# Optimization experiments

Measured on AMD Instinct MI355X. Metric: run time of the kernel, lower is better.

Reference implementation:

```python
import jax, jax.numpy as jnp
import numpy as np


def setup_inputs() -> dict:
    key = jax.random.key(0)
    k1, k2, k3 = jax.random.split(key, 3)
    N, M, D = 8192, 8192, 128
    feat = jax.random.normal(k1, (N, D), dtype=jnp.float32)
    feat2 = jax.random.normal(k2, (M, D), dtype=jnp.float32)
    labels = jax.random.randint(k3, (N,), 0, M, dtype=jnp.int64)
    temp = jnp.array(1.0, dtype=jnp.float32)
    return {"feat": feat, "feat2": feat2, "temp": temp, "labels": labels}


def reference(feat, feat2, temp, labels):
    # (same math as sqrt(sum((x[:,None]-y)**2, -1)) but without the N*M*D intermediate).
    x_sq = jnp.sum(feat * feat, axis=-1)    # [N]
    y_sq = jnp.sum(feat2 * feat2, axis=-1)  # [M]
    sq_dist = x_sq[:, None] + y_sq[None, :] - 2.0 * (feat @ feat2.T)  # [N, M]
    dist = jnp.sqrt(jnp.maximum(sq_dist, 0.0))
    logits = -temp * dist                    # [N, M]
    # Cross-entropy with mean reduction (nn.CrossEntropyLoss default)
    log_z = jax.nn.logsumexp(logits, axis=-1)                              # [N]
    picked = jnp.take_along_axis(logits, labels[:, None], axis=1)[:, 0]   # [N]
    return jnp.mean(log_z - picked)
```

## Files before the change

kernel.cpp:

```cpp
#include <hip/hip_runtime.h>
#include <hip/hip_bf16.h>
#include <stdint.h>

#define NR 8192
#define MC 8192
#define DD 128
#define MSPLIT 16
#define CPB 512
#define TILES 16
#define ROWBLK 128

typedef __attribute__((ext_vector_type(8))) short short8;
typedef __attribute__((ext_vector_type(16))) float f32x16;

__device__ __forceinline__ ushort bf16r(float f) {
    __hip_bfloat16 h = __float2bfloat16(f);
    return *(ushort*)&h;
}

__device__ __forceinline__ void gload_lds16(const void* g, void* l) {
    __builtin_amdgcn_global_load_lds(
        (const __attribute__((address_space(1))) uint32_t*)g,
        (__attribute__((address_space(3))) uint32_t*)l, 16, 0, 0);
}
__device__ __forceinline__ void gload_lds4(const void* g, void* l) {
    __builtin_amdgcn_global_load_lds(
        (const __attribute__((address_space(1))) uint32_t*)g,
        (__attribute__((address_space(3))) uint32_t*)l, 4, 0, 0);
}

__global__ __launch_bounds__(256) void prep_kernel(
    const float* __restrict__ feat, const float* __restrict__ feat2,
    const float* __restrict__ temp_p, const int* __restrict__ labels,
    ushort* __restrict__ fb, ushort* __restrict__ f2bf,
    float* __restrict__ xsq2, float* __restrict__ ysq2,
    float* __restrict__ pick, float* __restrict__ consts) {
    int b = blockIdx.x;
    if (b < 2048) {
        int row = b * 4 + (threadIdx.x >> 6);
        int l = threadIdx.x & 63;
        float temp = *temp_p;
        float c = temp * 1.4426950408889634f;
        float c2 = c * c;
        int lab = labels[row];
        float2 x = ((const float2*)(feat  + (size_t)row * DD))[l];
        float2 y = ((const float2*)(feat2 + (size_t)row * DD))[l];
        float2 z = ((const float2*)(feat2 + (size_t)lab * DD))[l];
        ushort2 ux; ux.x = bf16r(x.x); ux.y = bf16r(x.y);
        ((ushort2*)(fb + (size_t)row * DD))[l] = ux;
        float sx = x.x * x.x + x.y * x.y;
        float sy = y.x * y.x + y.y * y.y;
        float d0 = x.x - z.x, d1 = x.y - z.y;
        float sd = d0 * d0 + d1 * d1;
        #pragma unroll
        for (int off = 1; off < 64; off <<= 1) {
            sx += __shfl_xor(sx, off);
            sy += __shfl_xor(sy, off);
            sd += __shfl_xor(sd, off);
        }
        if (l == 0) {
            xsq2[row] = c2 * sx;
            ysq2[row] = c2 * sy;
            pick[row] = temp * __builtin_amdgcn_sqrtf(sd);
            if (row == 0) consts[0] = -2.0f * c2;
        }
    } else {
        int id = (b - 2048) * 256 + threadIdx.x;
        int slot = id & 63;
        int ks = (id >> 6) & 7;
        int tile = id >> 9;
        int col = tile * 32 + (slot & 31);
        int k0 = ks * 16 + (slot >> 5) * 8;
        const float* src = feat2 + (size_t)col * DD + k0;
        float4 v0 = ((const float4*)src)[0];
        float4 v1 = ((const float4*)src)[1];
        short8 o;
        o[0] = (short)bf16r(v0.x); o[1] = (short)bf16r(v0.y);
        o[2] = (short)bf16r(v0.z); o[3] = (short)bf16r(v0.w);
        o[4] = (short)bf16r(v1.x); o[5] = (short)bf16r(v1.y);
        o[6] = (short)bf16r(v1.z); o[7] = (short)bf16r(v1.w);
        ((short8*)f2bf)[id] = o;
    }
}

__global__ __launch_bounds__(256, 4) void main_kernel(
    const ushort* __restrict__ fb, const ushort* __restrict__ f2bf,
    const float* __restrict__ xsq2, const float* __restrict__ ysq2,
    const float* __restrict__ consts, float* __restrict__ spart) {
    __shared__ ushort lds[4][8 * 512];
    __shared__ float ys_lds[CPB];

    int bid = blockIdx.x;
    int cs = bid & (MSPLIT - 1);
    int rb = bid >> 4;
    int tid = threadIdx.x;
    int wave = tid >> 6, lane = tid & 63;
    int lcol = lane & 31, lhalf = lane >> 5;
    int rowbase = rb * ROWBLK + wave * 32;
    int tile0 = cs * TILES;
    float m2c2 = consts[0];

    short8 a[8];
    const ushort* ap = fb + (size_t)(rowbase + lcol) * DD + lhalf * 8;
    #pragma unroll
    for (int ks = 0; ks < 8; ++ks) a[ks] = *(const short8*)(ap + ks * 16);

    float xs2[16];
    #pragma unroll
    for (int r = 0; r < 16; ++r)
        xs2[r] = xsq2[rowbase + (r & 3) + 8 * (r >> 2) + 4 * lhalf];

    float s[16];
    #pragma unroll
    for (int r = 0; r < 16; ++r) s[r] = 0.f;

    {
        const float* ysrc = ysq2 + cs * CPB;
        gload_lds4(ysrc + wave * 64 + lane, &ys_lds[wave * 64]);
        gload_lds4(ysrc + (wave + 4) * 64 + lane, &ys_lds[(wave + 4) * 64]);
    }
    #pragma unroll
    for (int t0 = 0; t0 < 2; ++t0) {
        const ushort* g = f2bf + ((size_t)(tile0 + t0) * 8 + wave) * 512 + lane * 8;
        gload_lds16(g, &lds[t0][wave * 512]);
        gload_lds16(g + 4 * 512, &lds[t0][(wave + 4) * 512]);
    }

    #pragma unroll 1
    for (int t = 0; t < TILES; ++t) {
        if (t + 2 < TILES) {
            const ushort* g = f2bf + ((size_t)(tile0 + t + 2) * 8 + wave) * 512 + lane * 8;
            gload_lds16(g, &lds[(t + 2) & 3][wave * 512]);
            gload_lds16(g + 4 * 512, &lds[(t + 2) & 3][(wave + 4) * 512]);
            asm volatile("s_waitcnt vmcnt(4)" ::: "memory");
        } else if (t + 1 < TILES) {
            asm volatile("s_waitcnt vmcnt(2)" ::: "memory");
        } else {
            asm volatile("s_waitcnt vmcnt(0)" ::: "memory");
        }
        __builtin_amdgcn_s_barrier();

        float ysv = ys_lds[t * 32 + lcol];
        const ushort* lb = &lds[t & 3][0];
        f32x16 acc;
        #pragma unroll
        for (int r = 0; r < 16; ++r) acc[r] = 0.f;
        #pragma unroll
        for (int ks = 0; ks < 8; ++ks) {
            short8 bf = *(const short8*)(lb + ks * 512 + lane * 8);
            acc = __builtin_amdgcn_mfma_f32_32x32x16_bf16(a[ks], bf, acc, 0, 0, 0);
        }
        #pragma unroll
        for (int r = 0; r < 16; ++r) {
            float q = fmaxf(fmaf(m2c2, acc[r], xs2[r] + ysv), 0.f);
            s[r] += __builtin_amdgcn_exp2f(-__builtin_amdgcn_sqrtf(q));
        }
    }

    #pragma unroll
    for (int off = 1; off <= 16; off <<= 1)
        #pragma unroll
        for (int r = 0; r < 16; ++r) s[r] += __shfl_xor(s[r], off);

    if (lcol == 0) {
        float* sp = spart + (size_t)cs * NR + rowbase;
        #pragma unroll
        for (int r = 0; r < 16; ++r)
            sp[(r & 3) + 8 * (r >> 2) + 4 * lhalf] = s[r];
    }
}

__global__ __launch_bounds__(256) void finish1_kernel(
    const float* __restrict__ spart, const float* __restrict__ pick,
    float* __restrict__ partial) {
    __shared__ float red[4];
    int row = blockIdx.x * 256 + threadIdx.x;
    float ssum = 0.f;
    #pragma unroll
    for (int ms = 0; ms < MSPLIT; ++ms) ssum += spart[(size_t)ms * NR + row];
    float v = __builtin_amdgcn_logf(ssum) * 0.6931471805599453f + pick[row];
    #pragma unroll
    for (int off = 1; off < 64; off <<= 1) v += __shfl_xor(v, off);
    if ((threadIdx.x & 63) == 0) red[threadIdx.x >> 6] = v;
    __syncthreads();
    if (threadIdx.x == 0) partial[blockIdx.x] = red[0] + red[1] + red[2] + red[3];
}

__global__ void finish2_kernel(const float* __restrict__ partial, float* __restrict__ out) {
    float v = (threadIdx.x < 32) ? partial[threadIdx.x] : 0.f;
    #pragma unroll
    for (int off = 1; off < 64; off <<= 1) v += __shfl_xor(v, off);
    if (threadIdx.x == 0) out[0] = v * (1.0f / NR);
}

extern "C" void kernel_launch(void* const* d_in, const int* in_sizes, int n_in,
                              void* d_out, int out_size, void* d_ws, size_t ws_size,
                              hipStream_t stream) {
    const float* feat   = (const float*)d_in[0];
    const float* feat2  = (const float*)d_in[1];
    const float* temp   = (const float*)d_in[2];
    const int*   labels = (const int*)d_in[3];
    float* out = (float*)d_out;

    char* ws = (char*)d_ws;
    ushort* fb    = (ushort*)ws;
    ushort* f2bf  = (ushort*)(ws + (2u << 20));
    float*  xsq2  = (float*)(ws + (4u << 20));
    float*  ysq2  = xsq2 + NR;
    float*  pick  = ysq2 + MC;
    float*  consts  = pick + NR;
    float*  partial = consts + 16;
    float*  spart = (float*)(ws + (5u << 20));

    prep_kernel<<<2560, 256, 0, stream>>>(feat, feat2, temp, labels,
                                          fb, f2bf, xsq2, ysq2, pick, consts);
    main_kernel<<<(NR / ROWBLK) * MSPLIT, 256, 0, stream>>>(fb, f2bf, xsq2, ysq2, consts, spart);
    finish1_kernel<<<NR / 256, 256, 0, stream>>>(spart, pick, partial);
    finish2_kernel<<<1, 64, 0, stream>>>(partial, out);
}
```

Baseline: 44.02 us.

## Fuse final reductions into main kernel via last-block atomic; process two tiles per iteration

Removes the two finish kernels: each main-kernel block bumps an atomic counter after writing its partial sums, and the last block to finish does the logsumexp reduction and writes the output. The spart layout becomes row-major so that block can read the 16 splits per row with float4 loads. The tile loop also now handles two tiles per barrier with two independent MFMA accumulators, waiting on vmcnt(0) and issuing the next pair of prefetches after the barrier. This trades two kernel launches and finer-grained load/compute overlap for a serial tail reduction in one block and atomic/fence overhead.

```diff
diff --git a/kernel.cpp b/kernel.cpp
--- a/kernel.cpp
+++ b/kernel.cpp
@@ -9,6 +9,7 @@
 #define CPB 512
 #define TILES 16
 #define ROWBLK 128
+#define GRID ((NR / ROWBLK) * MSPLIT)
 
 typedef __attribute__((ext_vector_type(8))) short short8;
 typedef __attribute__((ext_vector_type(16))) float f32x16;
@@ -34,8 +35,9 @@
     const float* __restrict__ temp_p, const int* __restrict__ labels,
     ushort* __restrict__ fb, ushort* __restrict__ f2bf,
     float* __restrict__ xsq2, float* __restrict__ ysq2,
-    float* __restrict__ pick, float* __restrict__ consts) {
+    float* __restrict__ pick, float* __restrict__ consts, int* __restrict__ done) {
     int b = blockIdx.x;
+    if (b == 0 && threadIdx.x == 0) *done = 0;
     if (b < 2048) {
         int row = b * 4 + (threadIdx.x >> 6);
         int l = threadIdx.x & 63;
@@ -86,9 +88,12 @@
 __global__ __launch_bounds__(256, 4) void main_kernel(
     const ushort* __restrict__ fb, const ushort* __restrict__ f2bf,
     const float* __restrict__ xsq2, const float* __restrict__ ysq2,
-    const float* __restrict__ consts, float* __restrict__ spart) {
+    const float* __restrict__ consts, float* __restrict__ spart,
+    const float* __restrict__ pick, int* __restrict__ done, float* __restrict__ out) {
     __shared__ ushort lds[4][8 * 512];
     __shared__ float ys_lds[CPB];
+    __shared__ float red[4];
+    __shared__ int last_flag;
 
     int bid = blockIdx.x;
     int cs = bid & (MSPLIT - 1);
@@ -118,42 +123,54 @@
         const float* ysrc = ysq2 + cs * CPB;
         gload_lds4(ysrc + wave * 64 + lane, &ys_lds[wave * 64]);
         gload_lds4(ysrc + (wave + 4) * 64 + lane, &ys_lds[(wave + 4) * 64]);
-    }
-    #pragma unroll
-    for (int t0 = 0; t0 < 2; ++t0) {
-        const ushort* g = f2bf + ((size_t)(tile0 + t0) * 8 + wave) * 512 + lane * 8;
-        gload_lds16(g, &lds[t0][wave * 512]);
-        gload_lds16(g + 4 * 512, &lds[t0][(wave + 4) * 512]);
+        #pragma unroll
+        for (int t0 = 0; t0 < 2; ++t0) {
+            const ushort* g = f2bf + ((size_t)(tile0 + t0) * 8 + wave) * 512 + lane * 8;
+            gload_lds16(g, &lds[t0][wave * 512]);
+            gload_lds16(g + 4 * 512, &lds[t0][(wave + 4) * 512]);
+        }
     }
 
     #pragma unroll 1
-    for (int t = 0; t < TILES; ++t) {
-        if (t + 2 < TILES) {
-            const ushort* g = f2bf + ((size_t)(tile0 + t + 2) * 8 + wave) * 512 + lane * 8;
-            gload_lds16(g, &lds[(t + 2) & 3][wave * 512]);
-            gload_lds16(g + 4 * 512, &lds[(t + 2) & 3][(wave + 4) * 512]);
-            asm volatile("s_waitcnt vmcnt(4)" ::: "memory");
-        } else if (t + 1 < TILES) {
-            asm volatile("s_waitcnt vmcnt(2)" ::: "memory");
-        } else {
-            asm volatile("s_waitcnt vmcnt(0)" ::: "memory");
-        }
+    for (int j = 0; j < TILES / 2; ++j) {
+        asm volatile("s_waitcnt vmcnt(0)" ::: "memory");
         __builtin_amdgcn_s_barrier();
 
-        float ysv = ys_lds[t * 32 + lcol];
-        const ushort* lb = &lds[t & 3][0];
-        f32x16 acc;
-        #pragma unroll
-        for (int r = 0; r < 16; ++r) acc[r] = 0.f;
+        if (j + 1 < TILES / 2) {
+            #pragma unroll
+            for (int p = 0; p < 2; ++p) {
+                int t = 2 * j + 2 + p;
+                const ushort* g = f2bf + ((size_t)(tile0 + t) * 8 + wave) * 512 + lane * 8;
+                gload_lds16(g, &lds[t & 3][wave * 512]);
+                gload_lds16(g + 4 * 512, &lds[t & 3][(wave + 4) * 512]);
+            }
+        }
+
+        int t0 = 2 * j, t1 = 2 * j + 1;
+        float ysv0 = ys_lds[t0 * 32 + lcol];
+        float ysv1 = ys_lds[t1 * 32 + lcol];
+        const ushort* lb0 = &lds[t0 & 3][0];
+        const ushort* lb1 = &lds[t1 & 3][0];
+
+        f32x16 acc0, acc1;
+        #pragma unroll
+        for (int r = 0; r < 16; ++r) { acc0[r] = 0.f; acc1[r] = 0.f; }
         #pragma unroll
         for (int ks = 0; ks < 8; ++ks) {
-            short8 bf = *(const short8*)(lb + ks * 512 + lane * 8);
-            acc = __builtin_amdgcn_mfma_f32_32x32x16_bf16(a[ks], bf, acc, 0, 0, 0);
+            short8 b0 = *(const short8*)(lb0 + ks * 512 + lane * 8);
+            acc0 = __builtin_amdgcn_mfma_f32_32x32x16_bf16(a[ks], b0, acc0, 0, 0, 0);
+        }
+        #pragma unroll
+        for (int ks = 0; ks < 8; ++ks) {
+            short8 b1 = *(const short8*)(lb1 + ks * 512 + lane * 8);
+            acc1 = __builtin_amdgcn_mfma_f32_32x32x16_bf16(a[ks], b1, acc1, 0, 0, 0);
         }
         #pragma unroll
         for (int r = 0; r < 16; ++r) {
-            float q = fmaxf(fmaf(m2c2, acc[r], xs2[r] + ysv), 0.f);
-            s[r] += __builtin_amdgcn_exp2f(-__builtin_amdgcn_sqrtf(q));
+            float q0 = fmaxf(fmaf(m2c2, acc0[r], xs2[r] + ysv0), 0.f);
+            float q1 = fmaxf(fmaf(m2c2, acc1[r], xs2[r] + ysv1), 0.f);
+            s[r] += __builtin_amdgcn_exp2f(-__builtin_amdgcn_sqrtf(q0));
+            s[r] += __builtin_amdgcn_exp2f(-__builtin_amdgcn_sqrtf(q1));
         }
     }
 
@@ -163,34 +180,35 @@
         for (int r = 0; r < 16; ++r) s[r] += __shfl_xor(s[r], off);
 
     if (lcol == 0) {
-        float* sp = spart + (size_t)cs * NR + rowbase;
         #pragma unroll
         for (int r = 0; r < 16; ++r)
-            sp[(r & 3) + 8 * (r >> 2) + 4 * lhalf] = s[r];
-    }
-}
-
-__global__ __launch_bounds__(256) void finish1_kernel(
-    const float* __restrict__ spart, const float* __restrict__ pick,
-    float* __restrict__ partial) {
-    __shared__ float red[4];
-    int row = blockIdx.x * 256 + threadIdx.x;
-    float ssum = 0.f;
-    #pragma unroll
-    for (int ms = 0; ms < MSPLIT; ++ms) ssum += spart[(size_t)ms * NR + row];
-    float v = __builtin_amdgcn_logf(ssum) * 0.6931471805599453f + pick[row];
-    #pragma unroll
-    for (int off = 1; off < 64; off <<= 1) v += __shfl_xor(v, off);
-    if ((threadIdx.x & 63) == 0) red[threadIdx.x >> 6] = v;
+            spart[(size_t)(rowbase + (r & 3) + 8 * (r >> 2) + 4 * lhalf) * MSPLIT + cs] = s[r];
+    }
+
+    __threadfence();
+    if (tid == 0) last_flag = (atomicAdd(done, 1) == GRID - 1);
     __syncthreads();
-    if (threadIdx.x == 0) partial[blockIdx.x] = red[0] + red[1] + red[2] + red[3];
-}
-
-__global__ void finish2_kernel(const float* __restrict__ partial, float* __restrict__ out) {
-    float v = (threadIdx.x < 32) ? partial[threadIdx.x] : 0.f;
-    #pragma unroll
-    for (int off = 1; off < 64; off <<= 1) v += __shfl_xor(v, off);
-    if (threadIdx.x == 0) out[0] = v * (1.0f / NR);
+    if (!last_flag) return;
+    __threadfence();
+
+    float local = 0.f;
+    #pragma unroll 1
+    for (int k = 0; k < NR / 256; ++k) {
+        int row = k * 256 + tid;
+        const float4* sp = (const float4*)(spart + (size_t)row * MSPLIT);
+        float4 p0 = sp[0], p1 = sp[1], p2 = sp[2], p3 = sp[3];
+        float ssum = (((((((((((((((p0.x + p0.y) + p0.z) + p0.w) + p1.x) + p1.y) + p1.z)
+                     + p1.w) + p2.x) + p2.y) + p2.z) + p2.w) + p3.x) + p3.y) + p3.z) + p3.w);
+        local += __builtin_amdgcn_logf(ssum) * 0.6931471805599453f + pick[row];
+    }
+    #pragma unroll
+    for (int off = 1; off < 64; off <<= 1) local += __shfl_xor(local, off);
+    if ((tid & 63) == 0) red[tid >> 6] = local;
+    __syncthreads();
+    if (tid == 0) {
+        out[0] = (red[0] + red[1] + red[2] + red[3]) * (1.0f / NR);
+        *done = 0;
+    }
 }
 
 extern "C" void kernel_launch(void* const* d_in, const int* in_sizes, int n_in,
@@ -209,12 +227,11 @@
     float*  ysq2  = xsq2 + NR;
     float*  pick  = ysq2 + MC;
     float*  consts  = pick + NR;
-    float*  partial = consts + 16;
+    int*    done    = (int*)(consts + 16);
     float*  spart = (float*)(ws + (5u << 20));
 
     prep_kernel<<<2560, 256, 0, stream>>>(feat, feat2, temp, labels,
-                                          fb, f2bf, xsq2, ysq2, pick, consts);
-    main_kernel<<<(NR / ROWBLK) * MSPLIT, 256, 0, stream>>>(fb, f2bf, xsq2, ysq2, consts, spart);
-    finish1_kernel<<<NR / 256, 256, 0, stream>>>(spart, pick, partial);
-    finish2_kernel<<<1, 64, 0, stream>>>(partial, out);
-}
+                                          fb, f2bf, xsq2, ysq2, pick, consts, done);
+    main_kernel<<<GRID, 256, 0, stream>>>(fb, f2bf, xsq2, ysq2, consts, spart,
+                                          pick, done, out);
+}
```

After: 140.5 us. +219.2%, slower.

## Shrink main kernel blocks to two waves with double-buffered B tiles

Applied to the files above, without the earlier changes.

Halves the row block to 64 rows and the main kernel block to 128 threads, which doubles the grid and halves LDS per block. The four-deep prefetch ring becomes a two-buffer scheme: each iteration waits for all loads, hits a barrier, then issues the next tile. Wave priority is raised around the MFMA loop, and the clamp to zero before sqrt becomes an fabs. The aim is more resident blocks and better latency hiding from extra parallelism, but each B tile is now reloaded by twice as many blocks and the prefetch lead is shorter.

```diff
diff --git a/kernel.cpp b/kernel.cpp
--- a/kernel.cpp
+++ b/kernel.cpp
@@ -8,7 +8,8 @@
 #define MSPLIT 16
 #define CPB 512
 #define TILES 16
-#define ROWBLK 128
+#define ROWBLK 64
+#define GRID ((NR / ROWBLK) * MSPLIT)
 
 typedef __attribute__((ext_vector_type(8))) short short8;
 typedef __attribute__((ext_vector_type(16))) float f32x16;
@@ -83,11 +84,11 @@
     }
 }
 
-__global__ __launch_bounds__(256, 4) void main_kernel(
+__global__ __launch_bounds__(128, 4) void main_kernel(
     const ushort* __restrict__ fb, const ushort* __restrict__ f2bf,
     const float* __restrict__ xsq2, const float* __restrict__ ysq2,
     const float* __restrict__ consts, float* __restrict__ spart) {
-    __shared__ ushort lds[4][8 * 512];
+    __shared__ ushort lds[2][8 * 512];
     __shared__ float ys_lds[CPB];
 
     int bid = blockIdx.x;
@@ -116,44 +117,48 @@
 
     {
         const float* ysrc = ysq2 + cs * CPB;
-        gload_lds4(ysrc + wave * 64 + lane, &ys_lds[wave * 64]);
-        gload_lds4(ysrc + (wave + 4) * 64 + lane, &ys_lds[(wave + 4) * 64]);
-    }
-    #pragma unroll
-    for (int t0 = 0; t0 < 2; ++t0) {
-        const ushort* g = f2bf + ((size_t)(tile0 + t0) * 8 + wave) * 512 + lane * 8;
-        gload_lds16(g, &lds[t0][wave * 512]);
-        gload_lds16(g + 4 * 512, &lds[t0][(wave + 4) * 512]);
+        #pragma unroll
+        for (int c = 0; c < 4; ++c) {
+            int ch = wave * 4 + c;
+            gload_lds4(ysrc + ch * 64 + lane, &ys_lds[ch * 64]);
+        }
+        #pragma unroll
+        for (int c = 0; c < 4; ++c) {
+            int ch = wave * 4 + c;
+            gload_lds16(f2bf + ((size_t)tile0 * 8 + ch) * 512 + lane * 8,
+                        &lds[0][ch * 512]);
+        }
     }
 
     #pragma unroll 1
     for (int t = 0; t < TILES; ++t) {
-        if (t + 2 < TILES) {
-            const ushort* g = f2bf + ((size_t)(tile0 + t + 2) * 8 + wave) * 512 + lane * 8;
-            gload_lds16(g, &lds[(t + 2) & 3][wave * 512]);
-            gload_lds16(g + 4 * 512, &lds[(t + 2) & 3][(wave + 4) * 512]);
-            asm volatile("s_waitcnt vmcnt(4)" ::: "memory");
-        } else if (t + 1 < TILES) {
-            asm volatile("s_waitcnt vmcnt(2)" ::: "memory");
-        } else {
-            asm volatile("s_waitcnt vmcnt(0)" ::: "memory");
-        }
+        asm volatile("s_waitcnt vmcnt(0)" ::: "memory");
         __builtin_amdgcn_s_barrier();
+        if (t + 1 < TILES) {
+            #pragma unroll
+            for (int c = 0; c < 4; ++c) {
+                int ch = wave * 4 + c;
+                gload_lds16(f2bf + ((size_t)(tile0 + t + 1) * 8 + ch) * 512 + lane * 8,
+                            &lds[(t + 1) & 1][ch * 512]);
+            }
+        }
 
         float ysv = ys_lds[t * 32 + lcol];
-        const ushort* lb = &lds[t & 3][0];
+        const ushort* lb = &lds[t & 1][0];
         f32x16 acc;
         #pragma unroll
         for (int r = 0; r < 16; ++r) acc[r] = 0.f;
+        __builtin_amdgcn_s_setprio(1);
         #pragma unroll
         for (int ks = 0; ks < 8; ++ks) {
             short8 bf = *(const short8*)(lb + ks * 512 + lane * 8);
             acc = __builtin_amdgcn_mfma_f32_32x32x16_bf16(a[ks], bf, acc, 0, 0, 0);
         }
+        __builtin_amdgcn_s_setprio(0);
         #pragma unroll
         for (int r = 0; r < 16; ++r) {
-            float q = fmaxf(fmaf(m2c2, acc[r], xs2[r] + ysv), 0.f);
-            s[r] += __builtin_amdgcn_exp2f(-__builtin_amdgcn_sqrtf(q));
+            float q = fmaf(m2c2, acc[r], xs2[r] + ysv);
+            s[r] += __builtin_amdgcn_exp2f(-__builtin_amdgcn_sqrtf(__builtin_fabsf(q)));
         }
     }
 
@@ -214,7 +219,7 @@
 
     prep_kernel<<<2560, 256, 0, stream>>>(feat, feat2, temp, labels,
                                           fb, f2bf, xsq2, ysq2, pick, consts);
-    main_kernel<<<(NR / ROWBLK) * MSPLIT, 256, 0, stream>>>(fb, f2bf, xsq2, ysq2, consts, spart);
+    main_kernel<<<GRID, 128, 0, stream>>>(fb, f2bf, xsq2, ysq2, consts, spart);
     finish1_kernel<<<NR / 256, 256, 0, stream>>>(spart, pick, partial);
     finish2_kernel<<<1, 64, 0, stream>>>(partial, out);
 }
```

Measured after the change: 45.03 us. 2.3% more time.
